# Performance work log

Measured on AMD Instinct MI355X. Metric: run time of the kernel, lower is better.

## Reference

```python
import jax, jax.numpy as jnp
import numpy as np

DIM=2048; NH=16; QK_NOPE=128; QK_ROPE=64; QK_HD=QK_NOPE+QK_ROPE; V_HD=128
Q_LORA=1536; KV_LORA=512
IDX_NH=16; IDX_HD=128; IDX_TOPK=1024
B=1; S=2048
NEG=-1e30  # finite stand-in for -inf mask

def _hadamard(n):
    H=np.array([[1.0]],dtype=np.float32)
    while H.shape[0]<n:
        H=np.block([[H,H],[H,-H]])
    return H
_H=jnp.asarray(_hadamard(IDX_HD),jnp.bfloat16)  # symmetric Sylvester Hadamard

def _rope_tables(s,d):
    inv=1.0/(10000.0**(np.arange(0,d,2)/float(d)))
    ang=np.outer(np.arange(s),inv)
    return jnp.asarray(np.cos(ang),jnp.float32),jnp.asarray(np.sin(ang),jnp.float32)

def _rope_interleaved(x,cos,sin):
    # pairs (x[2i], x[2i+1]); x: (b,s,h,d), cos/sin: (s,d//2)
    x1=x[...,0::2]; x2=x[...,1::2]
    c=cos[None,:,None,:]; s_=sin[None,:,None,:]
    return jnp.stack([x1*c-x2*s_,x1*s_+x2*c],axis=-1).reshape(x.shape)

def _rope_half(x,cos,sin):
    # non-interleaved: pairs (x[i], x[i+d/2])
    d=x.shape[-1]//2
    x1=x[...,:d]; x2=x[...,d:]
    c=cos[None,:,None,:]; s_=sin[None,:,None,:]
    return jnp.concatenate([x1*c-x2*s_,x1*s_+x2*c],axis=-1)

def _rms(x,w,eps=1e-6):
    xf=x.astype(jnp.float32)
    xf=xf*jax.lax.rsqrt(jnp.mean(xf*xf,axis=-1,keepdims=True)+eps)
    return (w*xf).astype(x.dtype)

def _ln(x,w,b,eps=1e-6):
    xf=x.astype(jnp.float32)
    mu=jnp.mean(xf,axis=-1,keepdims=True)
    var=jnp.mean((xf-mu)**2,axis=-1,keepdims=True)
    return ((xf-mu)*jax.lax.rsqrt(var+eps)*w+b).astype(x.dtype)

def _rotate(x):
    # rotate_activation: bf16 Hadamard transform, x @ H * d^-0.5 (H symmetric)
    return (x.astype(jnp.bfloat16)@_H)*(IDX_HD**-0.5)

def _forward(x,start_pos,freqs_cos,freqs_sin,mask,q_a_proj,q_a_ln_w,q_b_proj,kv_a_proj,kv_a_ln_w,kv_b_proj,o_proj,idx_wq_b,idx_wk,idx_knorm_w,idx_knorm_b,idx_weights_proj):
    b,s,_=x.shape  # start_pos==0 prefill -> cache slice == current k/kv
    sm_scale=QK_HD**-0.5
    qr=_rms(x@q_a_proj.T,q_a_ln_w)                       # (b,s,q_lora)
    q=(qr@q_b_proj.T).reshape(b,s,NH,QK_HD)
    q_nope=q[...,:QK_NOPE]
    q_pe=_rope_interleaved(q[...,QK_NOPE:],freqs_cos,freqs_sin)
    kvp=x@kv_a_proj.T
    kv=_rms(kvp[...,:KV_LORA],kv_a_ln_w)                 # latent kv cache (b,t,c)
    k_pe=_rope_interleaved(kvp[...,KV_LORA:][:,:,None,:],freqs_cos,freqs_sin)[:,:,0,:]
    # ---------- Indexer ----------
    iq=(qr@idx_wq_b.T).reshape(b,s,IDX_NH,IDX_HD)
    iq=jnp.concatenate([_rope_half(iq[...,:QK_ROPE],freqs_cos,freqs_sin),iq[...,QK_ROPE:]],axis=-1)
    ik=_ln(x@idx_wk.T,idx_knorm_w,idx_knorm_b)           # (b,s,IDX_HD)
    ik=jnp.concatenate([_rope_half(ik[:,:,None,:QK_ROPE],freqs_cos,freqs_sin)[:,:,0,:],ik[...,QK_ROPE:]],axis=-1)
    iq=_rotate(iq); ik=_rotate(ik)                       # bf16 Hadamard-rotated
    iw=(x@idx_weights_proj.T)*(IDX_NH**-0.5)             # (b,s,hI)
    wq=(iw[...,None]*iq.astype(jnp.float32)*(IDX_HD**-0.5)).astype(jnp.bfloat16)
    sc=jnp.einsum('bshd,btd->bsht',wq,ik,preferred_element_type=jnp.float32)
    index_score=jax.nn.relu(sc).sum(axis=2)+mask[None]   # bf16_index: relu, head-sum
    _,topk=jax.lax.top_k(index_score,min(IDX_TOPK,s))    # (b,s,K)
    imask=jnp.full((b,s,s),jnp.float32(NEG))
    imask=imask.at[jnp.arange(b)[:,None,None],jnp.arange(s)[None,:,None],topk].set(0.0)
    imask=imask+mask[None]
    # ---------- Latent attention (absorbed) ----------
    wkv=kv_b_proj.reshape(NH,QK_NOPE+V_HD,KV_LORA)
    q_abs=jnp.einsum('bshd,hdc->bshc',q_nope,wkv[:,:QK_NOPE])
    scores=(jnp.einsum('bshc,btc->bsht',q_abs,kv)+jnp.einsum('bshr,btr->bsht',q_pe,k_pe))*sm_scale
    scores=scores+imask[:,:,None,:]
    p=jax.nn.softmax(scores.astype(jnp.float32),axis=-1).astype(x.dtype)
    o=jnp.einsum('bsht,btc->bshc',p,kv)
    o=jnp.einsum('bshc,hdc->bshd',o,wkv[:,QK_NOPE:])
    return o.reshape(b,s,NH*V_HD)@o_proj.T

def setup_inputs():
    key=jax.random.key(0)
    ks=jax.random.split(key,10)
    def w(k,shape):
        return jax.random.normal(k,shape,jnp.float32)*(shape[-1]**-0.5)
    cos,sin=_rope_tables(S,QK_ROPE)
    causal=jnp.where(jnp.triu(jnp.ones((S,S),bool),1),jnp.float32(NEG),jnp.float32(0.0))
    return {
        'x':jax.random.normal(ks[0],(B,S,DIM),jnp.float32),
        'start_pos':0,
        'freqs_cos':cos,'freqs_sin':sin,'mask':causal,
        'q_a_proj':w(ks[1],(Q_LORA,DIM)),
        'q_a_ln_w':jnp.ones((Q_LORA,),jnp.float32),
        'q_b_proj':w(ks[2],(NH*QK_HD,Q_LORA)),
        'kv_a_proj':w(ks[3],(KV_LORA+QK_ROPE,DIM)),
        'kv_a_ln_w':jnp.ones((KV_LORA,),jnp.float32),
        'kv_b_proj':w(ks[4],(NH*(QK_NOPE+V_HD),KV_LORA)),
        'o_proj':w(ks[5],(DIM,NH*V_HD)),
        'idx_wq_b':w(ks[6],(IDX_NH*IDX_HD,Q_LORA)),
        'idx_wk':w(ks[7],(IDX_HD,DIM)),
        'idx_knorm_w':jnp.ones((IDX_HD,),jnp.float32),
        'idx_knorm_b':jnp.zeros((IDX_HD,),jnp.float32),
        'idx_weights_proj':w(ks[8],(IDX_NH,DIM)),
    }

def reference(x,start_pos,freqs_cos,freqs_sin,mask,q_a_proj,q_a_ln_w,q_b_proj,kv_a_proj,kv_a_ln_w,kv_b_proj,o_proj,idx_wq_b,idx_wk,idx_knorm_w,idx_knorm_b,idx_weights_proj):
    return _forward(x,start_pos,freqs_cos,freqs_sin,mask,q_a_proj,q_a_ln_w,q_b_proj,kv_a_proj,kv_a_ln_w,kv_b_proj,o_proj,idx_wq_b,idx_wk,idx_knorm_w,idx_knorm_b,idx_weights_proj)
```

## Files before the change

### kernel.cpp

```cpp
#include <hip/hip_runtime.h>
#include <hip/hip_bf16.h>
#include <math.h>

#define S 2048
#define NH 16
#define DIM 2048
#define QK_NOPE 128
#define QK_ROPE 64
#define QK_HD 192
#define V_HD 128
#define Q_LORA 1536
#define KV_LORA 512
#define IDX_HD 128
#define SM_SCALE 0.07216878364870323f
#define SCHUNK 512
#define PADK 40
#define XPLD 2256
#define QLD 5120
#define XPLD_PAD 2304

typedef __hip_bfloat16 bf16;
typedef unsigned short ushort_t;
typedef __attribute__((ext_vector_type(8))) short short8;
typedef __attribute__((ext_vector_type(4))) float f32x4;

__device__ __forceinline__ f32x4 mfma_bf16(short8 a, short8 b, f32x4 c) {
    return __builtin_amdgcn_mfma_f32_16x16x32_bf16(a, b, c, 0, 0, 0);
}
__device__ __forceinline__ void async16(const void* g, void* l) {
    __builtin_amdgcn_global_load_lds((const __attribute__((address_space(1))) void*)g,
                                     (__attribute__((address_space(3))) void*)l, 16, 0, 0);
}
__device__ __forceinline__ unsigned short f2bf(float f) {
    unsigned int u = __float_as_uint(f);
    return (unsigned short)((u + 0x7fff + ((u >> 16) & 1)) >> 16);
}
__device__ __forceinline__ float bf2f(unsigned short b) {
    return __uint_as_float(((unsigned int)b) << 16);
}

__global__ __launch_bounds__(256) void split_kernel(const float* __restrict__ in, ushort_t* __restrict__ hi,
                                                    ushort_t* __restrict__ lo, int n4) {
    int idx = blockIdx.x * 256 + threadIdx.x;
    if (idx >= n4) return;
    float4 v = ((const float4*)in)[idx];
    ushort4 h, l;
    h.x = f2bf(v.x); l.x = f2bf(v.x - bf2f(h.x));
    h.y = f2bf(v.y); l.y = f2bf(v.y - bf2f(h.y));
    h.z = f2bf(v.z); l.z = f2bf(v.z - bf2f(h.z));
    h.w = f2bf(v.w); l.w = f2bf(v.w - bf2f(h.w));
    ((ushort4*)hi)[idx] = h;
    ((ushort4*)lo)[idx] = l;
}

__global__ __launch_bounds__(256) void splitw2_kernel(const float* __restrict__ kv_b,
                                                      ushort_t* __restrict__ w2h, ushort_t* __restrict__ w2l) {
    int idx = blockIdx.x * 256 + threadIdx.x;
    int h = idx >> 14, rem = idx & 16383;
    int row = rem >> 7, c4 = (rem & 127) * 4;
    float4 v = *(const float4*)(kv_b + ((size_t)(h * 256 + 128 + row)) * 512 + c4);
    ushort4 hh, ll;
    hh.x = f2bf(v.x); ll.x = f2bf(v.x - bf2f(hh.x));
    hh.y = f2bf(v.y); ll.y = f2bf(v.y - bf2f(hh.y));
    hh.z = f2bf(v.z); ll.z = f2bf(v.z - bf2f(hh.z));
    hh.w = f2bf(v.w); ll.w = f2bf(v.w - bf2f(hh.w));
    *(ushort4*)(w2h + ((size_t)(h * 128 + row)) * 512 + c4) = hh;
    *(ushort4*)(w2l + ((size_t)(h * 128 + row)) * 512 + c4) = ll;
}

__global__ __launch_bounds__(256) void gemm3_lds(const ushort_t* __restrict__ Ah, const ushort_t* __restrict__ Al,
                                                 const ushort_t* __restrict__ Bh, const ushort_t* __restrict__ Bl,
                                                 float* __restrict__ C, int M, int N, int K) {
    __shared__ ushort_t sAh[128 * 32], sAl[128 * 32], sBh[128 * 32], sBl[128 * 32];
    const int tid = threadIdx.x;
    const int bm = blockIdx.y * 128, bn = blockIdx.x * 128;
    const int w = tid >> 6, lane = tid & 63;
    const int wm = (w >> 1) * 64, wn = (w & 1) * 64;
    const int fr = lane & 15, fk = (lane >> 4) * 8;
    const int srow = tid >> 2, skc = (tid & 3) * 8;
    f32x4 acc[4][4];
    for (int i = 0; i < 4; ++i)
        for (int j = 0; j < 4; ++j) acc[i][j] = f32x4{0.f, 0.f, 0.f, 0.f};
    const ushort_t* pAh0 = Ah + (size_t)(bm + srow) * K + skc;
    const ushort_t* pAh1 = Ah + (size_t)(bm + 64 + srow) * K + skc;
    const ushort_t* pAl0 = Al + (size_t)(bm + srow) * K + skc;
    const ushort_t* pAl1 = Al + (size_t)(bm + 64 + srow) * K + skc;
    const ushort_t* pBh0 = Bh + (size_t)(bn + srow) * K + skc;
    const ushort_t* pBh1 = Bh + (size_t)(bn + 64 + srow) * K + skc;
    const ushort_t* pBl0 = Bl + (size_t)(bn + srow) * K + skc;
    const ushort_t* pBl1 = Bl + (size_t)(bn + 64 + srow) * K + skc;
    ushort_t* dA0 = &sAh[srow * 32 + skc];
    ushort_t* dA1 = &sAh[(64 + srow) * 32 + skc];
    ushort_t* dAl0 = &sAl[srow * 32 + skc];
    ushort_t* dAl1 = &sAl[(64 + srow) * 32 + skc];
    ushort_t* dB0 = &sBh[srow * 32 + skc];
    ushort_t* dB1 = &sBh[(64 + srow) * 32 + skc];
    ushort_t* dBl0 = &sBl[srow * 32 + skc];
    ushort_t* dBl1 = &sBl[(64 + srow) * 32 + skc];
    for (int k0 = 0; k0 < K; k0 += 32) {
        __syncthreads();
        async16(pAh0, dA0);  async16(pAh1, dA1);
        async16(pAl0, dAl0); async16(pAl1, dAl1);
        async16(pBh0, dB0);  async16(pBh1, dB1);
        async16(pBl0, dBl0); async16(pBl1, dBl1);
        pAh0 += 32; pAh1 += 32; pAl0 += 32; pAl1 += 32;
        pBh0 += 32; pBh1 += 32; pBl0 += 32; pBl1 += 32;
        __syncthreads();
        short8 ahf[4], alf[4], bhf[4], blf[4];
        for (int i = 0; i < 4; ++i) {
            int ro = (wm + i * 16 + fr) * 32 + fk;
            ahf[i] = *(const short8*)&sAh[ro];
            alf[i] = *(const short8*)&sAl[ro];
        }
        for (int j = 0; j < 4; ++j) {
            int ro = (wn + j * 16 + fr) * 32 + fk;
            bhf[j] = *(const short8*)&sBh[ro];
            blf[j] = *(const short8*)&sBl[ro];
        }
        for (int i = 0; i < 4; ++i)
            for (int j = 0; j < 4; ++j) {
                acc[i][j] = mfma_bf16(ahf[i], bhf[j], acc[i][j]);
                acc[i][j] = mfma_bf16(ahf[i], blf[j], acc[i][j]);
                acc[i][j] = mfma_bf16(alf[i], bhf[j], acc[i][j]);
            }
    }
    const int cr = (lane >> 4) * 4, cc = lane & 15;
    for (int i = 0; i < 4; ++i)
        for (int j = 0; j < 4; ++j) {
            int row = bm + wm + i * 16 + cr;
            int col = bn + wn + j * 16 + cc;
            if (col < N)
                for (int r = 0; r < 4; ++r)
                    C[(size_t)(row + r) * N + col] = acc[i][j][r];
        }
}

__global__ __launch_bounds__(256) void rms_kernel(const float* __restrict__ in, float* __restrict__ out,
                                                  const float* __restrict__ w, int C, int ldin, int ldout) {
    const int row = blockIdx.x;
    const float* xr = in + (size_t)row * ldin;
    float* yr = out + (size_t)row * ldout;
    float ss = 0.f;
    for (int c = threadIdx.x; c < C; c += 256) { float v = xr[c]; ss += v * v; }
    for (int o = 32; o; o >>= 1) ss += __shfl_down(ss, o, 64);
    __shared__ float red[4];
    const int wave = threadIdx.x >> 6, lane = threadIdx.x & 63;
    if (lane == 0) red[wave] = ss;
    __syncthreads();
    const float tot = red[0] + red[1] + red[2] + red[3];
    const float scale = rsqrtf(tot / (float)C + 1e-6f);
    for (int c = threadIdx.x; c < C; c += 256) yr[c] = w[c] * (xr[c] * scale);
}

__global__ __launch_bounds__(256) void rms_split_kernel(const float* __restrict__ in, ushort_t* __restrict__ hi,
                                                        ushort_t* __restrict__ lo, const float* __restrict__ w,
                                                        int C, int ldin) {
    const int row = blockIdx.x;
    const float* xr = in + (size_t)row * ldin;
    float ss = 0.f;
    for (int c = threadIdx.x; c < C; c += 256) { float v = xr[c]; ss += v * v; }
    for (int o = 32; o; o >>= 1) ss += __shfl_down(ss, o, 64);
    __shared__ float red[4];
    const int wave = threadIdx.x >> 6, lane = threadIdx.x & 63;
    if (lane == 0) red[wave] = ss;
    __syncthreads();
    const float tot = red[0] + red[1] + red[2] + red[3];
    const float scale = rsqrtf(tot / (float)C + 1e-6f);
    for (int c = threadIdx.x; c < C; c += 256) {
        float v = w[c] * (xr[c] * scale);
        unsigned short h = f2bf(v);
        hi[(size_t)row * C + c] = h;
        lo[(size_t)row * C + c] = f2bf(v - bf2f(h));
    }
}

__global__ __launch_bounds__(128) void ln_kernel(float* __restrict__ x, const float* __restrict__ w,
                                                 const float* __restrict__ b, int ld) {
    const int row = blockIdx.x;
    float* xr = x + (size_t)row * ld;
    const int tid = threadIdx.x;
    float v = xr[tid];
    float sm = v;
    for (int o = 32; o; o >>= 1) sm += __shfl_down(sm, o, 64);
    __shared__ float red[2];
    if ((tid & 63) == 0) red[tid >> 6] = sm;
    __syncthreads();
    const float mu = (red[0] + red[1]) * (1.f / 128.f);
    __syncthreads();
    float d = v - mu;
    float sv = d * d;
    for (int o = 32; o; o >>= 1) sv += __shfl_down(sv, o, 64);
    if ((tid & 63) == 0) red[tid >> 6] = sv;
    __syncthreads();
    const float var = (red[0] + red[1]) * (1.f / 128.f);
    const float rs = rsqrtf(var + 1e-6f);
    xr[tid] = (v - mu) * rs * w[tid] + b[tid];
}

__global__ __launch_bounds__(256) void rope_inter_kernel(float* __restrict__ X, const float* __restrict__ ct,
                                                         const float* __restrict__ st, int H, int hs, int off,
                                                         int ld) {
    int idx = blockIdx.x * 256 + threadIdx.x;
    int k = idx & 31;
    int h = (idx >> 5) % H;
    int s = idx / (32 * H);
    if (s >= S) return;
    float c = ct[s * 32 + k], sn = st[s * 32 + k];
    float* p = X + (size_t)s * ld + h * hs + off;
    float x1 = p[2 * k], x2 = p[2 * k + 1];
    p[2 * k]     = x1 * c - x2 * sn;
    p[2 * k + 1] = x1 * sn + x2 * c;
}

__global__ __launch_bounds__(256) void rope_half_kernel(float* __restrict__ X, const float* __restrict__ ct,
                                                        const float* __restrict__ st, int H, int hs, int ld,
                                                        int soff) {
    int idx = blockIdx.x * 256 + threadIdx.x;
    int k = idx & 31;
    int h = (idx >> 5) % H;
    int s = idx / (32 * H) + soff;
    if (s >= S) return;
    float c = ct[s * 32 + k], sn = st[s * 32 + k];
    float* p = X + (size_t)s * ld + h * hs;
    float x1 = p[k], x2 = p[32 + k];
    p[k]      = x1 * c - x2 * sn;
    p[32 + k] = x1 * sn + x2 * c;
}

__global__ __launch_bounds__(128) void rotate_kernel(const float* __restrict__ in, int lds, int H,
                                                     bf16* __restrict__ out, int roff) {
    __shared__ float xs[128];
    const int r = blockIdx.x + roff, j = threadIdx.x;
    const int s = r / H, h = r - s * H;
    float v = in[(size_t)s * lds + h * 128 + j];
    xs[j] = __bfloat162float(__float2bfloat16(v));
    __syncthreads();
    float acc = 0.f;
    for (int d = 0; d < 128; ++d) {
        float xv = xs[d];
        acc += (__popc(d & j) & 1) ? -xv : xv;
    }
    float t = __bfloat162float(__float2bfloat16(acc)) * 0.08838834764831845f;
    out[(size_t)r * 128 + j] = __float2bfloat16(t);
}

__global__ __launch_bounds__(256) void wq_kernel(const float* __restrict__ iwb, bf16* __restrict__ iqr,
                                                 int ioff) {
    int idx = blockIdx.x * 256 + threadIdx.x + ioff;
    int s = idx >> 11, h = (idx >> 7) & 15;
    float a = 0.25f * iwb[(size_t)s * XPLD + h];
    float v = __bfloat162float(iqr[idx]);
    float t = (a * v) * 0.08838834764831845f;
    iqr[idx] = __float2bfloat16(t);
}

__global__ __launch_bounds__(256) void iscore_mfma(const bf16* __restrict__ wq, const bf16* __restrict__ ik,
                                                   float* __restrict__ out) {
    if (blockIdx.x > blockIdx.y + 8) return;
    __shared__ unsigned short As[128 * 32], Bs[128 * 32];
    const int bs = (blockIdx.y + 8) * 128, bt = blockIdx.x * 128;
    const int tid = threadIdx.x, w = tid >> 6, lane = tid & 63;
    const int wm = (w >> 1) * 64, wn = (w & 1) * 64;
    const int fr = lane & 15, fk = (lane >> 4) * 8;
    const int srow = lane >> 2, skc = (lane & 3) * 8;
    f32x4 sum[4][4];
    for (int i = 0; i < 4; ++i)
        for (int j = 0; j < 4; ++j) sum[i][j] = f32x4{0.f, 0.f, 0.f, 0.f};
    for (int h = 0; h < 16; ++h) {
        f32x4 acc[4][4];
        for (int i = 0; i < 4; ++i)
            for (int j = 0; j < 4; ++j) acc[i][j] = f32x4{0.f, 0.f, 0.f, 0.f};
        for (int k0 = 0; k0 < 128; k0 += 32) {
            __syncthreads();
            for (int i = 0; i < 2; ++i) {
                int seg = i * 4 + w;
                async16(wq + (size_t)(bs + seg * 16 + srow) * 2048 + h * 128 + k0 + skc, &As[seg * 512]);
                async16(ik + (size_t)(bt + seg * 16 + srow) * 128 + k0 + skc, &Bs[seg * 512]);
            }
            __syncthreads();
            short8 af[4], bff[4];
            for (int i = 0; i < 4; ++i) af[i]  = *(const short8*)&As[(wm + i * 16 + fr) * 32 + fk];
            for (int j = 0; j < 4; ++j) bff[j] = *(const short8*)&Bs[(wn + j * 16 + fr) * 32 + fk];
            for (int i = 0; i < 4; ++i)
                for (int j = 0; j < 4; ++j)
                    acc[i][j] = mfma_bf16(af[i], bff[j], acc[i][j]);
        }
        for (int i = 0; i < 4; ++i)
            for (int j = 0; j < 4; ++j)
                for (int r = 0; r < 4; ++r)
                    sum[i][j][r] += fmaxf(acc[i][j][r], 0.f);
    }
    const int cr = (lane >> 4) * 4, cc = lane & 15;
    for (int i = 0; i < 4; ++i)
        for (int j = 0; j < 4; ++j)
            for (int r = 0; r < 4; ++r)
                out[(size_t)(bs + wm + i * 16 + cr + r) * 2048 + bt + wn + j * 16 + cc] = sum[i][j][r];
}

__global__ __launch_bounds__(256) void topk_kernel(const float* __restrict__ isc, int* __restrict__ tk,
                                                   int s0) {
    __shared__ unsigned long long keys[2048];
    const int s = s0 + blockIdx.x;
    const float* row = isc + (size_t)s * 2048;
    for (int t = threadIdx.x; t < 2048; t += 256) {
        unsigned long long kk = 0ull;
        if (t <= s) {
            unsigned int vb = __float_as_uint(row[t]);
            kk = ((unsigned long long)vb << 32) | (unsigned int)(2048 - t);
        }
        keys[t] = kk;
    }
    __syncthreads();
    for (int k = 2; k <= 2048; k <<= 1) {
        for (int j = k >> 1; j > 0; j >>= 1) {
            for (int t = threadIdx.x; t < 2048; t += 256) {
                int l = t ^ j;
                if (l > t) {
                    bool up = ((t & k) == 0);
                    unsigned long long a = keys[t], b = keys[l];
                    bool sw = up ? (a < b) : (a > b);
                    if (sw) { keys[t] = b; keys[l] = a; }
                }
            }
            __syncthreads();
        }
    }
    const int cnt = min(1024, s + 1);
    for (int i = threadIdx.x; i < 1024; i += 256) {
        int t = (i < cnt) ? (2048 - (int)(keys[i] & 0xFFFFFFFFull)) : -1;
        tk[(size_t)s * 1024 + i] = t;
    }
}

__global__ __launch_bounds__(256) void w1t_kernel(const float* __restrict__ kv_b, float* __restrict__ w1t) {
    __shared__ float ts[64][65];
    const int cb = blockIdx.x * 64, db = blockIdx.y * 64, h = blockIdx.z;
    const int t = threadIdx.x;
    for (int it = 0; it < 16; ++it) {
        int idx = it * 256 + t;
        int rr = idx >> 6, cc = idx & 63;
        ts[rr][cc] = kv_b[(size_t)(h * 256 + db + rr) * 512 + cb + cc];
    }
    __syncthreads();
    for (int it = 0; it < 16; ++it) {
        int idx = it * 256 + t;
        int rr = idx >> 6, cc = idx & 63;
        w1t[(size_t)h * 65536 + (size_t)(cb + rr) * 128 + db + cc] = ts[cc][rr];
    }
}

__global__ __launch_bounds__(576) void kvsplit_kernel(const float* __restrict__ kv, const float* __restrict__ kpe,
                                                      ushort_t* __restrict__ kvh, ushort_t* __restrict__ kvl,
                                                      unsigned int* __restrict__ kvi) {
    const int t = blockIdx.x, c = threadIdx.x;
    float v = (c < 512) ? kv[(size_t)t * 512 + c] : kpe[(size_t)t * XPLD + c];
    unsigned short hi = f2bf(v);
    unsigned short lo = f2bf(v - bf2f(hi));
    kvh[(size_t)t * 576 + c] = hi;
    kvl[(size_t)t * 576 + c] = lo;
    if (c < 512) kvi[(size_t)t * 512 + c] = (unsigned int)hi | ((unsigned int)lo << 16);
}

__global__ __launch_bounds__(256) void qabs_mfma(const float* __restrict__ q, const float* __restrict__ w1t,
                                                 ushort_t* __restrict__ qah, ushort_t* __restrict__ qal) {
    __shared__ unsigned short Ah[128 * PADK], Al[128 * PADK], Bh[128 * PADK], Bl[128 * PADK];
    const int tid = threadIdx.x;
    const int bn = blockIdx.x * 128, bm = blockIdx.y * 128, h = blockIdx.z;
    const int w = tid >> 6, lane = tid & 63;
    const int wm = (w >> 1) * 64, wn = (w & 1) * 64;
    const int fr = lane & 15, fk = (lane >> 4) * 8;
    f32x4 acc[4][4];
    for (int i = 0; i < 4; ++i)
        for (int j = 0; j < 4; ++j) acc[i][j] = f32x4{0.f, 0.f, 0.f, 0.f};
    for (int k0 = 0; k0 < 128; k0 += 32) {
        __syncthreads();
        for (int it = 0; it < 4; ++it) {
            int f = it * 256 + tid;
            int row = f >> 3, kc = (f & 7) * 4;
            float4 av = *(const float4*)(q + (size_t)(bm + row) * QLD + h * QK_HD + k0 + kc);
            float4 bv = *(const float4*)(w1t + (size_t)h * 65536 + (size_t)(bn + row) * 128 + k0 + kc);
            ushort4 ahi, alo, bhi, blo;
            ahi.x = f2bf(av.x); alo.x = f2bf(av.x - bf2f(ahi.x));
            ahi.y = f2bf(av.y); alo.y = f2bf(av.y - bf2f(ahi.y));
            ahi.z = f2bf(av.z); alo.z = f2bf(av.z - bf2f(ahi.z));
            ahi.w = f2bf(av.w); alo.w = f2bf(av.w - bf2f(ahi.w));
            bhi.x = f2bf(bv.x); blo.x = f2bf(bv.x - bf2f(bhi.x));
            bhi.y = f2bf(bv.y); blo.y = f2bf(bv.y - bf2f(bhi.y));
            bhi.z = f2bf(bv.z); blo.z = f2bf(bv.z - bf2f(bhi.z));
            bhi.w = f2bf(bv.w); blo.w = f2bf(bv.w - bf2f(bhi.w));
            *(ushort4*)&Ah[row * PADK + kc] = ahi;
            *(ushort4*)&Al[row * PADK + kc] = alo;
            *(ushort4*)&Bh[row * PADK + kc] = bhi;
            *(ushort4*)&Bl[row * PADK + kc] = blo;
        }
        __syncthreads();
        short8 ahf[4], alf[4], bhf[4], blf[4];
        for (int i = 0; i < 4; ++i) {
            int ro = (wm + i * 16 + fr) * PADK + fk;
            ahf[i] = *(const short8*)&Ah[ro];
            alf[i] = *(const short8*)&Al[ro];
        }
        for (int j = 0; j < 4; ++j) {
            int ro = (wn + j * 16 + fr) * PADK + fk;
            bhf[j] = *(const short8*)&Bh[ro];
            blf[j] = *(const short8*)&Bl[ro];
        }
        for (int i = 0; i < 4; ++i)
            for (int j = 0; j < 4; ++j) {
                acc[i][j] = mfma_bf16(ahf[i], bhf[j], acc[i][j]);
                acc[i][j] = mfma_bf16(ahf[i], blf[j], acc[i][j]);
                acc[i][j] = mfma_bf16(alf[i], bhf[j], acc[i][j]);
            }
    }
    const int cr = (lane >> 4) * 4, cc = lane & 15;
    for (int i = 0; i < 4; ++i)
        for (int j = 0; j < 4; ++j)
            for (int r = 0; r < 4; ++r) {
                int srow = bm + wm + i * 16 + cr + r;
                int col = bn + wn + j * 16 + cc;
                float f = acc[i][j][r] * SM_SCALE;
                size_t addr = ((size_t)srow * 16 + h) * 576 + col;
                unsigned short hi = f2bf(f);
                qah[addr] = hi;
                qal[addr] = f2bf(f - bf2f(hi));
            }
}

__global__ __launch_bounds__(256) void qpe_split(const float* __restrict__ q, ushort_t* __restrict__ qah,
                                                 ushort_t* __restrict__ qal) {
    int idx = blockIdx.x * 256 + threadIdx.x;
    int r = idx & 63, h = (idx >> 6) & 15, s = idx >> 10;
    float f = q[(size_t)s * QLD + h * QK_HD + 128 + r] * SM_SCALE;
    size_t addr = ((size_t)s * 16 + h) * 576 + 512 + r;
    unsigned short hi = f2bf(f);
    qah[addr] = hi;
    qal[addr] = f2bf(f - bf2f(hi));
}

#define SC_STAGE(BUF, O)                                    \
    async16(gha + (O), &kh[BUF][w * 1024]);                 \
    async16(ghb + (O), &kh[BUF][w * 1024 + 512]);           \
    async16(gla + (O), &kl[BUF][w * 1024]);                 \
    async16(glb + (O), &kl[BUF][w * 1024 + 512]);
__global__ __launch_bounds__(512) void attn_score_mfma(const ushort_t* __restrict__ qah,
                                                       const ushort_t* __restrict__ qal,
                                                       const ushort_t* __restrict__ kvh,
                                                       const ushort_t* __restrict__ kvl,
                                                       const int* __restrict__ tk,
                                                       float* __restrict__ scb, int s0, int dense) {
    const int sl = blockIdx.x, s = s0 + sl, pass = blockIdx.y;
    const int tid = threadIdx.x, w = tid >> 6, lane = tid & 63;
    const int cnt = min(1024, s + 1);
    if (pass * 256 >= cnt) {
        for (int i = tid; i < 4096; i += 512) {
            int head = i >> 8, key = i & 255;
            scb[((size_t)sl * 16 + head) * 1024 + pass * 256 + key] = -1e30f;
        }
        return;
    }
    __shared__ __align__(16) ushort_t kh[2][8192], kl[2][8192];
    const int rloc = lane >> 2;
    int t_a, t_b;
    if (dense) {
        t_a = pass * 256 + w * 32 + rloc;
        t_b = t_a + 16;
    } else {
        int ta = tk[(size_t)s * 1024 + pass * 256 + w * 32 + rloc];
        int tb = tk[(size_t)s * 1024 + pass * 256 + w * 32 + 16 + rloc];
        t_a = ta < 0 ? 0 : ta;
        t_b = tb < 0 ? 0 : tb;
    }
    const int swg = (lane & 3) ^ ((lane >> 3) & 3);
    const ushort_t* gha = kvh + (size_t)t_a * 576 + swg * 8;
    const ushort_t* ghb = kvh + (size_t)t_b * 576 + swg * 8;
    const ushort_t* gla = kvl + (size_t)t_a * 576 + swg * 8;
    const ushort_t* glb = kvl + (size_t)t_b * 576 + swg * 8;
    const int fr = lane & 15, g = lane >> 4;
    const size_t abase = ((size_t)s * 16 + fr) * 576 + g * 8;
    const int ro0 = w * 1024 + fr * 32 + ((g ^ ((fr >> 1) & 3)) << 3);
    const int ro1 = ro0 + 512;
    f32x4 acc0 = {0.f, 0.f, 0.f, 0.f}, acc1 = {0.f, 0.f, 0.f, 0.f};
    SC_STAGE(0, 0)
    short8 qh = *(const short8*)(qah + abase);
    short8 ql = *(const short8*)(qal + abase);
    for (int ch = 0; ch < 17; ++ch) {
        const int cur = ch & 1;
        SC_STAGE(cur ^ 1, (ch + 1) * 32)
        short8 qhn = *(const short8*)(qah + abase + (ch + 1) * 32);
        short8 qln = *(const short8*)(qal + abase + (ch + 1) * 32);
        asm volatile("s_waitcnt vmcnt(6)" ::: "memory");
        __builtin_amdgcn_sched_barrier(0);
        short8 bh0 = *(const short8*)&kh[cur][ro0];
        short8 bl0 = *(const short8*)&kl[cur][ro0];
        short8 bh1 = *(const short8*)&kh[cur][ro1];
        short8 bl1 = *(const short8*)&kl[cur][ro1];
        acc0 = mfma_bf16(qh, bh0, acc0);
        acc0 = mfma_bf16(qh, bl0, acc0);
        acc0 = mfma_bf16(ql, bh0, acc0);
        acc1 = mfma_bf16(qh, bh1, acc1);
        acc1 = mfma_bf16(qh, bl1, acc1);
        acc1 = mfma_bf16(ql, bh1, acc1);
        qh = qhn; ql = qln;
    }
    {
        asm volatile("s_waitcnt vmcnt(0)" ::: "memory");
        __builtin_amdgcn_sched_barrier(0);
        short8 bh0 = *(const short8*)&kh[1][ro0];
        short8 bl0 = *(const short8*)&kl[1][ro0];
        short8 bh1 = *(const short8*)&kh[1][ro1];
        short8 bl1 = *(const short8*)&kl[1][ro1];
        acc0 = mfma_bf16(qh, bh0, acc0);
        acc0 = mfma_bf16(qh, bl0, acc0);
        acc0 = mfma_bf16(ql, bh0, acc0);
        acc1 = mfma_bf16(qh, bh1, acc1);
        acc1 = mfma_bf16(qh, bl1, acc1);
        acc1 = mfma_bf16(ql, bh1, acc1);
    }
    const int cr = (lane >> 4) * 4, cc = lane & 15;
    for (int r = 0; r < 4; ++r) {
        int head = cr + r;
        int key0 = pass * 256 + w * 32 + cc;
        int key1 = key0 + 16;
        scb[((size_t)sl * 16 + head) * 1024 + key0] = (key0 < cnt) ? acc0[r] : -1e30f;
        scb[((size_t)sl * 16 + head) * 1024 + key1] = (key1 < cnt) ? acc1[r] : -1e30f;
    }
}

__global__ __launch_bounds__(256) void softmax_pb(const float* __restrict__ scb,
                                                  ushort_t* __restrict__ pbh, ushort_t* __restrict__ pbl) {
    const size_t row = blockIdx.x;
    const float* src = scb + row * 1024;
    const int tid = threadIdx.x, wave = tid >> 6, lane = tid & 63;
    __shared__ float red[4];
    float v[4];
    float m = -INFINITY;
    for (int i = 0; i < 4; ++i) { v[i] = src[tid + 256 * i]; m = fmaxf(m, v[i]); }
    for (int o = 32; o; o >>= 1) m = fmaxf(m, __shfl_down(m, o, 64));
    if (lane == 0) red[wave] = m;
    __syncthreads();
    m = fmaxf(fmaxf(red[0], red[1]), fmaxf(red[2], red[3]));
    __syncthreads();
    float e[4], l = 0.f;
    for (int i = 0; i < 4; ++i) { e[i] = __expf(v[i] - m); l += e[i]; }
    for (int o = 32; o; o >>= 1) l += __shfl_down(l, o, 64);
    if (lane == 0) red[wave] = l;
    __syncthreads();
    const float il = 1.f / (red[0] + red[1] + red[2] + red[3]);
    for (int i = 0; i < 4; ++i) {
        float p = e[i] * il;
        unsigned short hi = f2bf(p);
        pbh[row * 1024 + tid + 256 * i] = hi;
        pbl[row * 1024 + tid + 256 * i] = f2bf(p - bf2f(hi));
    }
}

#define PV_GATHER(KC)                                                                    \
    g0 = *(const uint4*)(kvi + (size_t)tks[(KC) * 32 + r0     ] * 512 + gp4);            \
    g1 = *(const uint4*)(kvi + (size_t)tks[(KC) * 32 + r0 + 4 ] * 512 + gp4);            \
    g2 = *(const uint4*)(kvi + (size_t)tks[(KC) * 32 + r0 + 8 ] * 512 + gp4);            \
    g3 = *(const uint4*)(kvi + (size_t)tks[(KC) * 32 + r0 + 12] * 512 + gp4);            \
    g4 = *(const uint4*)(kvi + (size_t)tks[(KC) * 32 + r0 + 16] * 512 + gp4);            \
    g5 = *(const uint4*)(kvi + (size_t)tks[(KC) * 32 + r0 + 20] * 512 + gp4);            \
    g6 = *(const uint4*)(kvi + (size_t)tks[(KC) * 32 + r0 + 24] * 512 + gp4);            \
    g7 = *(const uint4*)(kvi + (size_t)tks[(KC) * 32 + r0 + 28] * 512 + gp4);
#define PV_STORE()                                                                       \
    *(uint4*)&vt[(r0     ) * 512 + ((gp ^ 0) << 2)] = g0;                                \
    *(uint4*)&vt[(r0 + 4 ) * 512 + ((gp ^ 0) << 2)] = g1;                                \
    *(uint4*)&vt[(r0 + 8 ) * 512 + ((gp ^ 2) << 2)] = g2;                                \
    *(uint4*)&vt[(r0 + 12) * 512 + ((gp ^ 2) << 2)] = g3;                                \
    *(uint4*)&vt[(r0 + 16) * 512 + ((gp ^ 4) << 2)] = g4;                                \
    *(uint4*)&vt[(r0 + 20) * 512 + ((gp ^ 4) << 2)] = g5;                                \
    *(uint4*)&vt[(r0 + 24) * 512 + ((gp ^ 6) << 2)] = g6;                                \
    *(uint4*)&vt[(r0 + 28) * 512 + ((gp ^ 6) << 2)] = g7;
__global__ __launch_bounds__(512) void attn_pv_mfma(const ushort_t* __restrict__ pbh,
                                                    const ushort_t* __restrict__ pbl,
                                                    const unsigned int* __restrict__ kvi,
                                                    const int* __restrict__ tk,
                                                    ushort_t* __restrict__ o1h, ushort_t* __restrict__ o1l,
                                                    int s0, int dense) {
    const int sl = blockIdx.x, s = s0 + sl;
    const int tid = threadIdx.x, w = tid >> 6, lane = tid & 63;
    __shared__ int tks[1024];
    __shared__ unsigned int vt[32 * 512];
    for (int j = tid; j < 1024; j += 512) {
        if (dense) {
            tks[j] = j;
        } else {
            int t = tk[(size_t)s * 1024 + j];
            tks[j] = t < 0 ? 0 : t;
        }
    }
    const int fr = lane & 15, g = lane >> 4, fko = g * 8;
    const int r0 = tid >> 7;
    const int gp = tid & 127;
    const int gp4 = gp * 4;
    f32x4 acc[4];
    for (int i = 0; i < 4; ++i) acc[i] = f32x4{0.f, 0.f, 0.f, 0.f};
    const size_t pbase = ((size_t)sl * 16 + fr) * 1024 + fko;
    uint4 g0, g1, g2, g3, g4, g5, g6, g7;
    __syncthreads();
    PV_GATHER(0)
    PV_STORE()
    __syncthreads();
    for (int kc = 0; kc < 32; ++kc) {
        if (kc < 31) {
            PV_GATHER(kc + 1)
        }
        short8 ph = *(const short8*)(pbh + pbase + kc * 32);
        short8 pl = *(const short8*)(pbl + pbase + kc * 32);
        #pragma unroll
        for (int sub = 0; sub < 4; ++sub) {
            const int cb = (w * 64 + sub * 16 + fr) ^ (g << 3);
            short8 bh, bl;
            #pragma unroll
            for (int jj = 0; jj < 8; ++jj) {
                const unsigned int v = vt[(fko + jj) * 512 + cb];
                bh[jj] = (short)(v & 0xffffu);
                bl[jj] = (short)(v >> 16);
            }
            acc[sub] = mfma_bf16(ph, bh, acc[sub]);
            acc[sub] = mfma_bf16(pl, bh, acc[sub]);
            acc[sub] = mfma_bf16(ph, bl, acc[sub]);
        }
        __syncthreads();
        if (kc < 31) {
            PV_STORE()
            __syncthreads();
        }
    }
    const int cr = (lane >> 4) * 4, cc = lane & 15;
    for (int sub = 0; sub < 4; ++sub)
        for (int r = 0; r < 4; ++r) {
            int head = cr + r, c = w * 64 + sub * 16 + cc;
            float f = acc[sub][r];
            unsigned short hv = f2bf(f);
            size_t addr = ((size_t)sl * 16 + head) * 512 + c;
            o1h[addr] = hv;
            o1l[addr] = f2bf(f - bf2f(hv));
        }
}

__global__ __launch_bounds__(256) void outproj_mfma(const ushort_t* __restrict__ o1h,
                                                    const ushort_t* __restrict__ o1l,
                                                    const ushort_t* __restrict__ w2h,
                                                    const ushort_t* __restrict__ w2l,
                                                    ushort_t* __restrict__ o2h, ushort_t* __restrict__ o2l,
                                                    int s0) {
    __shared__ ushort_t sAh[128 * 32], sAl[128 * 32], sBh[128 * 32], sBl[128 * 32];
    const int tid = threadIdx.x;
    const int bm = blockIdx.x * 128, h = blockIdx.y;
    const int w = tid >> 6, lane = tid & 63;
    const int wm = (w >> 1) * 64, wn = (w & 1) * 64;
    const int fr = lane & 15, fk = (lane >> 4) * 8;
    const int srow = tid >> 2, skc = (tid & 3) * 8;
    f32x4 acc[4][4];
    for (int i = 0; i < 4; ++i)
        for (int j = 0; j < 4; ++j) acc[i][j] = f32x4{0.f, 0.f, 0.f, 0.f};
    const ushort_t* pAh0 = o1h + ((size_t)(bm + srow) * 16 + h) * 512 + skc;
    const ushort_t* pAh1 = o1h + ((size_t)(bm + 64 + srow) * 16 + h) * 512 + skc;
    const ushort_t* pAl0 = o1l + ((size_t)(bm + srow) * 16 + h) * 512 + skc;
    const ushort_t* pAl1 = o1l + ((size_t)(bm + 64 + srow) * 16 + h) * 512 + skc;
    const ushort_t* pBh0 = w2h + ((size_t)(h * 128 + srow)) * 512 + skc;
    const ushort_t* pBh1 = w2h + ((size_t)(h * 128 + 64 + srow)) * 512 + skc;
    const ushort_t* pBl0 = w2l + ((size_t)(h * 128 + srow)) * 512 + skc;
    const ushort_t* pBl1 = w2l + ((size_t)(h * 128 + 64 + srow)) * 512 + skc;
    ushort_t* dA0 = &sAh[srow * 32 + skc];
    ushort_t* dA1 = &sAh[(64 + srow) * 32 + skc];
    ushort_t* dAl0 = &sAl[srow * 32 + skc];
    ushort_t* dAl1 = &sAl[(64 + srow) * 32 + skc];
    ushort_t* dB0 = &sBh[srow * 32 + skc];
    ushort_t* dB1 = &sBh[(64 + srow) * 32 + skc];
    ushort_t* dBl0 = &sBl[srow * 32 + skc];
    ushort_t* dBl1 = &sBl[(64 + srow) * 32 + skc];
    for (int k0 = 0; k0 < 512; k0 += 32) {
        __syncthreads();
        async16(pAh0, dA0);  async16(pAh1, dA1);
        async16(pAl0, dAl0); async16(pAl1, dAl1);
        async16(pBh0, dB0);  async16(pBh1, dB1);
        async16(pBl0, dBl0); async16(pBl1, dBl1);
        pAh0 += 32; pAh1 += 32; pAl0 += 32; pAl1 += 32;
        pBh0 += 32; pBh1 += 32; pBl0 += 32; pBl1 += 32;
        __syncthreads();
        short8 ahf[4], alf[4], bhf[4], blf[4];
        for (int i = 0; i < 4; ++i) {
            int ro = (wm + i * 16 + fr) * 32 + fk;
            ahf[i] = *(const short8*)&sAh[ro];
            alf[i] = *(const short8*)&sAl[ro];
        }
        for (int j = 0; j < 4; ++j) {
            int ro = (wn + j * 16 + fr) * 32 + fk;
            bhf[j] = *(const short8*)&sBh[ro];
            blf[j] = *(const short8*)&sBl[ro];
        }
        for (int i = 0; i < 4; ++i)
            for (int j = 0; j < 4; ++j) {
                acc[i][j] = mfma_bf16(ahf[i], bhf[j], acc[i][j]);
                acc[i][j] = mfma_bf16(ahf[i], blf[j], acc[i][j]);
                acc[i][j] = mfma_bf16(alf[i], bhf[j], acc[i][j]);
            }
    }
    const int cr = (lane >> 4) * 4, cc = lane & 15;
    for (int i = 0; i < 4; ++i)
        for (int j = 0; j < 4; ++j)
            for (int r = 0; r < 4; ++r) {
                int srow2 = s0 + bm + wm + i * 16 + cr + r;
                int col = wn + j * 16 + cc;
                size_t addr = (size_t)srow2 * 2048 + h * 128 + col;
                float f = acc[i][j][r];
                unsigned short hv = f2bf(f);
                o2h[addr] = hv;
                o2l[addr] = f2bf(f - bf2f(hv));
            }
}

extern "C" void kernel_launch(void* const* d_in, const int* in_sizes, int n_in,
                              void* d_out, int out_size, void* d_ws, size_t ws_size,
                              hipStream_t stream) {
    const float* x         = (const float*)d_in[0];
    const float* fcos      = (const float*)d_in[2];
    const float* fsin      = (const float*)d_in[3];
    const float* q_a_proj  = (const float*)d_in[5];
    const float* q_a_ln_w  = (const float*)d_in[6];
    const float* q_b_proj  = (const float*)d_in[7];
    const float* kv_a_proj = (const float*)d_in[8];
    const float* kv_a_ln_w = (const float*)d_in[9];
    const float* kv_b      = (const float*)d_in[10];
    const float* o_proj    = (const float*)d_in[11];
    const float* idx_wq_b  = (const float*)d_in[12];
    const float* idx_wk    = (const float*)d_in[13];
    const float* iknw      = (const float*)d_in[14];
    const float* iknb      = (const float*)d_in[15];
    const float* idx_wp    = (const float*)d_in[16];
    float* out = (float*)d_out;

    char* ws = (char*)d_ws;
    size_t off = 0;
    auto alloc = [&](size_t bytes) {
        char* p = ws + off;
        off += (bytes + 255) & ~(size_t)255;
        return p;
    };
    float* xp  = (float*)alloc((size_t)S * XPLD * 4);
    ushort_t* qrh = (ushort_t*)alloc((size_t)S * Q_LORA * 2);
    ushort_t* qrl = (ushort_t*)alloc((size_t)S * Q_LORA * 2);
    float* qib = (float*)alloc((size_t)S * QLD * 4);
    char* RAt  = alloc(31457280);
    float* isc = (float*)RAt;
    bf16* iqr  = (bf16*)(RAt + 16777216);
    bf16* ikr  = (bf16*)(RAt + 16777216 + 8388608);
    ushort_t* xh = (ushort_t*)RAt;
    ushort_t* xl = xh + (size_t)S * DIM;
    ushort_t* wq2h = (ushort_t*)RAt;
    ushort_t* wq2l = wq2h + (size_t)5120 * Q_LORA;
    float* w1t = (float*)RAt;
    ushort_t* wpackh = (ushort_t*)qib;
    ushort_t* wpackl = wpackh + (size_t)XPLD_PAD * DIM;
    char* kvtail = RAt + (size_t)22 * 1024 * 1024;
    unsigned int* kvi = (unsigned int*)kvtail;
    ushort_t* w2h = (ushort_t*)(kvtail + (size_t)4 * 1024 * 1024);
    ushort_t* w2l = w2h + (size_t)16 * 128 * 512;
    const size_t CHUNK_BYTES = (size_t)SCHUNK * 16 * 1024 * 4 + (size_t)SCHUNK * 16 * 1024 * 2 * 2
                             + (size_t)SCHUNK * 16 * 512 * 4;
    if (off < CHUNK_BYTES) off = (CHUNK_BYTES + 255) & ~(size_t)255;
    int* tk        = (int*)alloc((size_t)S * 1024 * 4);
    float* kv      = (float*)alloc((size_t)S * KV_LORA * 4);
    ushort_t* o2h  = (ushort_t*)alloc((size_t)S * 2048 * 2);
    ushort_t* o2l  = (ushort_t*)alloc((size_t)S * 2048 * 2);
    ushort_t* qah  = (ushort_t*)alloc((size_t)S * 16 * 576 * 2);
    ushort_t* qal  = (ushort_t*)alloc((size_t)S * 16 * 576 * 2);
    ushort_t* kvh  = (ushort_t*)alloc((size_t)S * 576 * 2);
    ushort_t* kvl  = (ushort_t*)alloc((size_t)S * 576 * 2);
    float* scb    = (float*)ws;
    ushort_t* pbh = (ushort_t*)(ws + (size_t)SCHUNK * 16 * 1024 * 4);
    ushort_t* pbl = pbh + (size_t)SCHUNK * 16 * 1024;
    ushort_t* o1h = (ushort_t*)(ws + (size_t)SCHUNK * 16 * 1024 * 8);
    ushort_t* o1l = o1h + (size_t)SCHUNK * 16 * 512;
    ushort_t* oph = (ushort_t*)ws;
    ushort_t* opl = oph + (size_t)DIM * 2048;

    split_kernel<<<S * DIM / 1024, 256, 0, stream>>>(x, xh, xl, S * DIM / 4);
    split_kernel<<<Q_LORA * DIM / 1024, 256, 0, stream>>>(q_a_proj, wpackh, wpackl, Q_LORA * DIM / 4);
    split_kernel<<<576 * DIM / 1024, 256, 0, stream>>>(kv_a_proj, wpackh + (size_t)1536 * DIM,
                                                       wpackl + (size_t)1536 * DIM, 576 * DIM / 4);
    split_kernel<<<128 * DIM / 1024, 256, 0, stream>>>(idx_wk, wpackh + (size_t)2112 * DIM,
                                                       wpackl + (size_t)2112 * DIM, 128 * DIM / 4);
    split_kernel<<<16 * DIM / 1024, 256, 0, stream>>>(idx_wp, wpackh + (size_t)2240 * DIM,
                                                      wpackl + (size_t)2240 * DIM, 16 * DIM / 4);
    hipMemsetAsync(wpackh + (size_t)XPLD * DIM, 0, (size_t)(XPLD_PAD - XPLD) * DIM * 2, stream);
    hipMemsetAsync(wpackl + (size_t)XPLD * DIM, 0, (size_t)(XPLD_PAD - XPLD) * DIM * 2, stream);
    gemm3_lds<<<dim3((XPLD + 127) / 128, S / 128), 256, 0, stream>>>(xh, xl, wpackh, wpackl, xp, S, XPLD, DIM);
    rms_split_kernel<<<S, 256, 0, stream>>>(xp, qrh, qrl, q_a_ln_w, Q_LORA, XPLD);
    rms_kernel<<<S, 256, 0, stream>>>(xp + 1536, kv, kv_a_ln_w, KV_LORA, XPLD, KV_LORA);
    split_kernel<<<3072 * Q_LORA / 1024, 256, 0, stream>>>(q_b_proj, wq2h, wq2l, 3072 * Q_LORA / 4);
    split_kernel<<<2048 * Q_LORA / 1024, 256, 0, stream>>>(idx_wq_b, wq2h + (size_t)3072 * Q_LORA,
                                                           wq2l + (size_t)3072 * Q_LORA, 2048 * Q_LORA / 4);
    gemm3_lds<<<dim3(QLD / 128, S / 128), 256, 0, stream>>>(qrh, qrl, wq2h, wq2l, qib, S, QLD, Q_LORA);
    rope_inter_kernel<<<S * NH * 32 / 256, 256, 0, stream>>>(qib, fcos, fsin, NH, QK_HD, QK_NOPE, QLD);
    rope_inter_kernel<<<S * 32 / 256, 256, 0, stream>>>(xp + 1536, fcos, fsin, 1, 0, KV_LORA, XPLD);
    rope_half_kernel<<<S * NH * 32 / 512, 256, 0, stream>>>(qib + 3072, fcos, fsin, NH, 128, QLD, 1024);
    ln_kernel<<<S, 128, 0, stream>>>(xp + 2112, iknw, iknb, XPLD);
    rope_half_kernel<<<S * 32 / 256, 256, 0, stream>>>(xp + 2112, fcos, fsin, 1, 0, XPLD, 0);
    rotate_kernel<<<S * NH / 2, 128, 0, stream>>>(qib + 3072, QLD, NH, iqr, 1024 * NH);
    rotate_kernel<<<S, 128, 0, stream>>>(xp + 2112, XPLD, 1, ikr, 0);
    wq_kernel<<<S * NH * 128 / 512, 256, 0, stream>>>(xp + 2240, iqr, 1024 * NH * 128);
    iscore_mfma<<<dim3(16, 8), 256, 0, stream>>>(iqr, ikr, isc);
    topk_kernel<<<1024, 256, 0, stream>>>(isc, tk, 1024);
    w1t_kernel<<<dim3(8, 2, 16), 256, 0, stream>>>(kv_b, w1t);
    qabs_mfma<<<dim3(4, S / 128, 16), 256, 0, stream>>>(qib, w1t, qah, qal);
    qpe_split<<<S * NH * 64 / 256, 256, 0, stream>>>(qib, qah, qal);
    kvsplit_kernel<<<S, 576, 0, stream>>>(kv, xp + 1536, kvh, kvl, kvi);
    splitw2_kernel<<<1024, 256, 0, stream>>>(kv_b, w2h, w2l);
    for (int c = 0; c < 4; ++c) {
        int s0 = c * SCHUNK;
        int dense = (c < 2) ? 1 : 0;
        attn_score_mfma<<<dim3(SCHUNK, 4), 512, 0, stream>>>(qah, qal, kvh, kvl, tk, scb, s0, dense);
        softmax_pb<<<SCHUNK * 16, 256, 0, stream>>>(scb, pbh, pbl);
        attn_pv_mfma<<<SCHUNK, 512, 0, stream>>>(pbh, pbl, kvi, tk, o1h, o1l, s0, dense);
        outproj_mfma<<<dim3(4, 16), 256, 0, stream>>>(o1h, o1l, w2h, w2l, o2h, o2l, s0);
    }
    split_kernel<<<DIM * 2048 / 1024, 256, 0, stream>>>(o_proj, oph, opl, DIM * 2048 / 4);
    gemm3_lds<<<dim3(DIM / 128, S / 128), 256, 0, stream>>>(o2h, o2l, oph, opl, out, S, DIM, NH * V_HD);
}
```

Before: 1.512 ms.

## Replace async LDS double buffer with register-staged single buffer in score kernel

In the attention score kernel, the double-buffered asynchronous global-to-LDS copies are replaced by a single LDS buffer. The next K chunk is prefetched into registers and written to LDS after the current chunk's MFMAs. Each wave reads and writes only its own LDS region, so no block barrier is needed. The launch bound now also asks for more waves per SIMD. The aim is to halve LDS use and raise occupancy, at the cost of more vector registers and less prefetch distance than the async path.

```diff
diff --git a/kernel.cpp b/kernel.cpp
--- a/kernel.cpp
+++ b/kernel.cpp
@@ -437,12 +437,7 @@
     qal[addr] = f2bf(f - bf2f(hi));
 }
 
-#define SC_STAGE(BUF, O)                                    \
-    async16(gha + (O), &kh[BUF][w * 1024]);                 \
-    async16(ghb + (O), &kh[BUF][w * 1024 + 512]);           \
-    async16(gla + (O), &kl[BUF][w * 1024]);                 \
-    async16(glb + (O), &kl[BUF][w * 1024 + 512]);
-__global__ __launch_bounds__(512) void attn_score_mfma(const ushort_t* __restrict__ qah,
+__global__ __launch_bounds__(512, 6) void attn_score_mfma(const ushort_t* __restrict__ qah,
                                                        const ushort_t* __restrict__ qal,
                                                        const ushort_t* __restrict__ kvh,
                                                        const ushort_t* __restrict__ kvl,
@@ -458,7 +453,7 @@
         }
         return;
     }
-    __shared__ __align__(16) ushort_t kh[2][8192], kl[2][8192];
+    __shared__ __align__(16) ushort_t kh[8192], kl[8192];
     const int rloc = lane >> 2;
     int t_a, t_b;
     if (dense) {
@@ -479,42 +474,42 @@
     const size_t abase = ((size_t)s * 16 + fr) * 576 + g * 8;
     const int ro0 = w * 1024 + fr * 32 + ((g ^ ((fr >> 1) & 3)) << 3);
     const int ro1 = ro0 + 512;
+    const int wb = w * 1024 + lane * 8;
     f32x4 acc0 = {0.f, 0.f, 0.f, 0.f}, acc1 = {0.f, 0.f, 0.f, 0.f};
-    SC_STAGE(0, 0)
+    uint4 ga = *(const uint4*)gha;
+    uint4 gb = *(const uint4*)ghb;
+    uint4 gc = *(const uint4*)gla;
+    uint4 gd = *(const uint4*)glb;
     short8 qh = *(const short8*)(qah + abase);
     short8 ql = *(const short8*)(qal + abase);
-    for (int ch = 0; ch < 17; ++ch) {
-        const int cur = ch & 1;
-        SC_STAGE(cur ^ 1, (ch + 1) * 32)
-        short8 qhn = *(const short8*)(qah + abase + (ch + 1) * 32);
-        short8 qln = *(const short8*)(qal + abase + (ch + 1) * 32);
-        asm volatile("s_waitcnt vmcnt(6)" ::: "memory");
-        __builtin_amdgcn_sched_barrier(0);
-        short8 bh0 = *(const short8*)&kh[cur][ro0];
-        short8 bl0 = *(const short8*)&kl[cur][ro0];
-        short8 bh1 = *(const short8*)&kh[cur][ro1];
-        short8 bl1 = *(const short8*)&kl[cur][ro1];
+    *(uint4*)&kh[wb] = ga;  *(uint4*)&kh[wb + 512] = gb;
+    *(uint4*)&kl[wb] = gc;  *(uint4*)&kl[wb + 512] = gd;
+    for (int ch = 0; ch < 18; ++ch) {
+        short8 qhn, qln;
+        if (ch < 17) {
+            const int off = (ch + 1) * 32;
+            ga = *(const uint4*)(gha + off);
+            gb = *(const uint4*)(ghb + off);
+            gc = *(const uint4*)(gla + off);
+            gd = *(const uint4*)(glb + off);
+            qhn = *(const short8*)(qah + abase + off);
+            qln = *(const short8*)(qal + abase + off);
+        }
+        short8 bh0 = *(const short8*)&kh[ro0];
+        short8 bl0 = *(const short8*)&kl[ro0];
+        short8 bh1 = *(const short8*)&kh[ro1];
+        short8 bl1 = *(const short8*)&kl[ro1];
         acc0 = mfma_bf16(qh, bh0, acc0);
         acc0 = mfma_bf16(qh, bl0, acc0);
         acc0 = mfma_bf16(ql, bh0, acc0);
         acc1 = mfma_bf16(qh, bh1, acc1);
         acc1 = mfma_bf16(qh, bl1, acc1);
         acc1 = mfma_bf16(ql, bh1, acc1);
-        qh = qhn; ql = qln;
-    }
-    {
-        asm volatile("s_waitcnt vmcnt(0)" ::: "memory");
-        __builtin_amdgcn_sched_barrier(0);
-        short8 bh0 = *(const short8*)&kh[1][ro0];
-        short8 bl0 = *(const short8*)&kl[1][ro0];
-        short8 bh1 = *(const short8*)&kh[1][ro1];
-        short8 bl1 = *(const short8*)&kl[1][ro1];
-        acc0 = mfma_bf16(qh, bh0, acc0);
-        acc0 = mfma_bf16(qh, bl0, acc0);
-        acc0 = mfma_bf16(ql, bh0, acc0);
-        acc1 = mfma_bf16(qh, bh1, acc1);
-        acc1 = mfma_bf16(qh, bl1, acc1);
-        acc1 = mfma_bf16(ql, bh1, acc1);
+        if (ch < 17) {
+            *(uint4*)&kh[wb] = ga;  *(uint4*)&kh[wb + 512] = gb;
+            *(uint4*)&kl[wb] = gc;  *(uint4*)&kl[wb + 512] = gd;
+            qh = qhn; ql = qln;
+        }
     }
     const int cr = (lane >> 4) * 4, cc = lane & 15;
     for (int r = 0; r < 4; ++r) {
```

Result: no change. 1.527 ms (+0.9%).
